# Performance work log

Hardware: AMD Instinct MI355X
Metric: run time of the kernel (lower is better)

## Reference

```python
import jax, jax.numpy as jnp
import numpy as np


def _sepconv1x1(x, dw, pw, b):
    # SeparableConv2D with kernel=1: depthwise 1x1 = per-channel scale, then pointwise matmul
    return jnp.einsum('nhwc,cd->nhwd', x * dw, pw) + b


def setup_inputs() -> dict:
    key = jax.random.key(0)
    ks = jax.random.split(key, 12)
    N, H, W, C_in, C_red = 4, 64, 64, 256, 64
    s = 0.05  # small init so softmax logits are well-conditioned
    return {
        'feature_maps': jax.random.normal(ks[0], (N, H, W, C_in), jnp.float32),
        'global_channel_output': jax.random.normal(ks[1], (N, H, W, C_in), jnp.float32),
        'dw_q': jax.random.normal(ks[2], (C_in,), jnp.float32) * s,
        'pw_q': jax.random.normal(ks[3], (C_in, C_red), jnp.float32) * s,
        'b_q': jnp.zeros((C_red,), jnp.float32),
        'dw_k': jax.random.normal(ks[4], (C_in,), jnp.float32) * s,
        'pw_k': jax.random.normal(ks[5], (C_in, C_red), jnp.float32) * s,
        'b_k': jnp.zeros((C_red,), jnp.float32),
        'dw_v': jax.random.normal(ks[6], (C_in,), jnp.float32) * s,
        'pw_v': jax.random.normal(ks[7], (C_in, C_red), jnp.float32) * s,
        'b_v': jnp.zeros((C_red,), jnp.float32),
        'dw_a': jax.random.normal(ks[8], (C_red,), jnp.float32) * s,
        'pw_a': jax.random.normal(ks[9], (C_red, C_in), jnp.float32) * s,
        'b_a': jnp.zeros((C_in,), jnp.float32),
    }


def reference(feature_maps, global_channel_output,
              dw_q, pw_q, b_q, dw_k, pw_k, b_k, dw_v, pw_v, b_v,
              dw_a, pw_a, b_a):
    N, H, W, _ = feature_maps.shape
    q = _sepconv1x1(feature_maps, dw_q, pw_q, b_q)  # [N,H,W,Cr]
    k = _sepconv1x1(feature_maps, dw_k, pw_k, b_k)
    v = _sepconv1x1(feature_maps, dw_v, pw_v, b_v)
    Cr = q.shape[-1]
    q = q.reshape(N, H * W, Cr)
    k = k.reshape(N, H * W, Cr)
    v = v.reshape(N, H * W, Cr)
    # tf.matmul(key, query, transpose_b=True): scores[i,j] = key_i . query_j
    scores = jnp.einsum('nic,njc->nij', k, q)  # [N,HW,HW]
    scores = jax.nn.softmax(scores, axis=-1)
    # tf.matmul(value, scores, transpose_a=True) -> [N,Cr,HW]
    att = jnp.einsum('nic,nij->ncj', v, scores)
    # faithful raw reshape (as in the original TF code) from [N,Cr,HW] to [N,H,W,Cr]
    att = att.reshape(N, H, W, Cr)
    att = _sepconv1x1(att, dw_a, pw_a, b_a)  # [N,H,W,C_in]
    return global_channel_output * att + global_channel_output
```

## Files before the change

### kernel.cpp

```cpp
#include <hip/hip_runtime.h>
#include <hip/hip_bf16.h>

typedef __attribute__((ext_vector_type(8))) __bf16 bf16x8;
typedef __attribute__((ext_vector_type(2))) __bf16 bf16x2;
typedef __attribute__((ext_vector_type(4))) float floatx4;
typedef __attribute__((ext_vector_type(4))) unsigned short us4;
typedef __attribute__((ext_vector_type(8))) unsigned short us8;
typedef __attribute__((ext_vector_type(4))) short s16x4;
typedef __attribute__((ext_vector_type(2))) unsigned int uint2v;
typedef __attribute__((ext_vector_type(4))) unsigned int uint4v;

#define MFMA16(A, B, C) __builtin_amdgcn_mfma_f32_16x16x32_bf16((A), (B), (C), 0, 0, 0)
#define MFMA1K(A, B, C) __builtin_amdgcn_mfma_f32_16x16x16bf16_1k((A), (B), (C), 0, 0, 0)

#define LOG2E 1.44269504088896340736f

#if __has_builtin(__builtin_amdgcn_exp2f)
#define EXP2F(x) __builtin_amdgcn_exp2f(x)
#else
#define EXP2F(x) exp2f(x)
#endif

static __device__ __forceinline__ unsigned short f2bfbits(float f) {
    __hip_bfloat16 h = __float2bfloat16(f);
    union { __hip_bfloat16 h; unsigned short u; } cv;
    cv.h = h;
    return cv.u;
}
static __device__ __forceinline__ unsigned int rne32(float f) {
    unsigned int u = __builtin_bit_cast(unsigned int, f);
    return u + 0x7fffu + ((u >> 16) & 1u);
}
static __device__ __forceinline__ unsigned short rne16(float f) {
    return (unsigned short)(rne32(f) >> 16);
}

#if __has_builtin(__builtin_amdgcn_cvt_pk_bf16_f32)
static __device__ __forceinline__ s16x4 pack4(float e0, float e1, float e2, float e3) {
    bf16x2 lo = __builtin_amdgcn_cvt_pk_bf16_f32(e0, e1);
    bf16x2 hi = __builtin_amdgcn_cvt_pk_bf16_f32(e2, e3);
    uint2v u = {__builtin_bit_cast(unsigned int, lo), __builtin_bit_cast(unsigned int, hi)};
    return __builtin_bit_cast(s16x4, u);
}
static __device__ __forceinline__ bf16x8 cvt8(floatx4 a, floatx4 b) {
    bf16x2 p0 = __builtin_amdgcn_cvt_pk_bf16_f32(a[0], a[1]);
    bf16x2 p1 = __builtin_amdgcn_cvt_pk_bf16_f32(a[2], a[3]);
    bf16x2 p2 = __builtin_amdgcn_cvt_pk_bf16_f32(b[0], b[1]);
    bf16x2 p3 = __builtin_amdgcn_cvt_pk_bf16_f32(b[2], b[3]);
    uint4v u = {__builtin_bit_cast(unsigned int, p0), __builtin_bit_cast(unsigned int, p1),
                __builtin_bit_cast(unsigned int, p2), __builtin_bit_cast(unsigned int, p3)};
    return __builtin_bit_cast(bf16x8, u);
}
#else
static __device__ __forceinline__ s16x4 pack4(float e0, float e1, float e2, float e3) {
    unsigned int pa = __builtin_amdgcn_perm(rne32(e1), rne32(e0), 0x07060302u);
    unsigned int pb = __builtin_amdgcn_perm(rne32(e3), rne32(e2), 0x07060302u);
    uint2v u = {pa, pb};
    return __builtin_bit_cast(s16x4, u);
}
static __device__ __forceinline__ bf16x8 cvt8(floatx4 a, floatx4 b) {
    us8 u;
#pragma unroll
    for (int i = 0; i < 4; i++) { u[i] = rne16(a[i]); u[4 + i] = rne16(b[i]); }
    return __builtin_bit_cast(bf16x8, u);
}
#endif

static __device__ __forceinline__ bf16x8 load_bf8(const __hip_bfloat16* p) {
    return *reinterpret_cast<const bf16x8*>(p);
}
static __device__ __forceinline__ float bf2f(unsigned short u) {
    unsigned int w = ((unsigned int)u) << 16;
    return __builtin_bit_cast(float, w);
}

static __device__ __forceinline__ void gld16(const void* g, void* l) {
    __builtin_amdgcn_global_load_lds(
        (const __attribute__((address_space(1))) unsigned int*)g,
        (__attribute__((address_space(3))) unsigned int*)l, 16, 0, 0);
}


__global__ __launch_bounds__(256) void proj_qkv(
    const float* __restrict__ x,
    const float* __restrict__ dwq, const float* __restrict__ pwq,
    const float* __restrict__ dwk, const float* __restrict__ pwk,
    const float* __restrict__ dwv, const float* __restrict__ pwv,
    const float* __restrict__ bqp, const float* __restrict__ bkp,
    const float* __restrict__ bvp,
    __hip_bfloat16* __restrict__ qf, __hip_bfloat16* __restrict__ kf,
    __hip_bfloat16* __restrict__ vf)
{
    __shared__ __hip_bfloat16 wle[16384];
    int b = blockIdx.x;
    int p = b >> 8;
    int tg = b & 255;
    int tid = threadIdx.x;

    const float* dw = (p == 0) ? dwq : ((p == 1) ? dwk : dwv);
    const float* pw = (p == 0) ? pwq : ((p == 1) ? pwk : pwv);
    float scale = (p == 1) ? LOG2E : 1.0f;

    {
        float dwc = dw[tid];
#pragma unroll
        for (int k = 0; k < 64; k++) {
            int idx = (k * 256 + tid) ^ ((k & 7) << 3);
            wle[idx] = __float2bfloat16(dwc * pw[tid * 64 + k] * scale);
        }
    }
    __syncthreads();

    int wv = tid >> 6;
    int wid = tg * 4 + wv;
    int lane = tid & 63;
    int l15 = lane & 15, quad = lane >> 4;

    floatx4 acc[4];
#pragma unroll
    for (int t = 0; t < 4; t++) acc[t] = (floatx4){0.f, 0.f, 0.f, 0.f};

    const float* xrow = x + (wid * 16 + l15) * 256 + quad * 8;
#pragma unroll
    for (int ks = 0; ks < 8; ks++) {
        floatx4 xa = *reinterpret_cast<const floatx4*>(xrow + ks * 32);
        floatx4 xb = *reinterpret_cast<const floatx4*>(xrow + ks * 32 + 4);
        bf16x8 a = cvt8(xa, xb);
#pragma unroll
        for (int t = 0; t < 4; t++) {
            int j0 = ((t * 16 + l15) * 256 + ks * 32 + quad * 8) ^ ((l15 & 7) << 3);
            bf16x8 bfr = *reinterpret_cast<const bf16x8*>(&wle[j0]);
            acc[t] = MFMA16(a, bfr, acc[t]);
        }
    }
    if (p < 2) {
        __hip_bfloat16* dst = (p == 0) ? qf : kf;
        const float* bias = (p == 0) ? bqp : bkp;
        float bscale = (p == 1) ? LOG2E : 1.0f;
#pragma unroll
        for (int t = 0; t < 4; t++) {
            float bsv = bias[t * 16 + l15] * bscale;
            int off0 = wid * 1024 + (t >> 1) * 512 +
                       (((((t & 1) << 1) | (l15 >> 3)) * 16 + quad * 4) * 8) + (l15 & 7);
#pragma unroll
            for (int r = 0; r < 4; r++)
                dst[off0 + r * 8] = __float2bfloat16(acc[t][r] + bsv);
        }
    } else {
#pragma unroll
        for (int t = 0; t < 4; t++) {
            float bsv = bvp[t * 16 + l15];
            us4 pk;
#pragma unroll
            for (int r = 0; r < 4; r++) pk[r] = f2bfbits(acc[t][r] + bsv);
            *reinterpret_cast<us4*>(vf + (wid * 4 + t) * 256 + lane * 4) = pk;
        }
    }
}

#define P1STEP(B0, B1, B2, B3) do {                                        \
    floatx4 z = (floatx4){0.f, 0.f, 0.f, 0.f};                             \
    floatx4 sA0 = MFMA16(a1, (B1), MFMA16(a0, (B0), z));                   \
    floatx4 sA1 = MFMA16(a1, (B3), MFMA16(a0, (B2), z));                   \
    floatx4 sB0 = MFMA16(a3, (B1), MFMA16(a2, (B0), z));                   \
    floatx4 sB1 = MFMA16(a3, (B3), MFMA16(a2, (B2), z));                   \
    _Pragma("unroll")                                                      \
    for (int r = 0; r < 4; r++) {                                          \
        lsA[r] += EXP2F(sA0[r]) + EXP2F(sA1[r]);                           \
        lsB[r] += EXP2F(sB0[r]) + EXP2F(sB1[r]);                           \
    }                                                                      \
} while (0)

__global__ __launch_bounds__(512) void pass1_rl(
    const __hip_bfloat16* __restrict__ qf, const __hip_bfloat16* __restrict__ kf,
    float* __restrict__ rl)
{
    int itg0 = blockIdx.x * 2;
    int n = itg0 >> 8;
    int jw = threadIdx.x >> 6;
    int lane = threadIdx.x & 63;
    int l15 = lane & 15, quad = lane >> 4;

    const __hip_bfloat16* kp = kf + itg0 * 1024 + lane * 8;
    bf16x8 a0 = load_bf8(kp);
    bf16x8 a1 = load_bf8(kp + 512);
    bf16x8 a2 = load_bf8(kp + 1024);
    bf16x8 a3 = load_bf8(kp + 1536);

    floatx4 lsA = (floatx4){0.f, 0.f, 0.f, 0.f};
    floatx4 lsB = (floatx4){0.f, 0.f, 0.f, 0.f};
    const __hip_bfloat16* qp0 = qf + (n * 256 + jw * 32) * 1024 + lane * 8;

    bf16x8 s0b0 = load_bf8(qp0);
    bf16x8 s0b1 = load_bf8(qp0 + 512);
    bf16x8 s0b2 = load_bf8(qp0 + 1024);
    bf16x8 s0b3 = load_bf8(qp0 + 1536);
    bf16x8 s1b0 = load_bf8(qp0 + 2048);
    bf16x8 s1b1 = load_bf8(qp0 + 2560);
    bf16x8 s1b2 = load_bf8(qp0 + 3072);
    bf16x8 s1b3 = load_bf8(qp0 + 3584);

    for (int it = 0; it < 16; it += 2) {
        bf16x8 n0 = load_bf8(qp0 + 4096);
        bf16x8 n1 = load_bf8(qp0 + 4608);
        bf16x8 n2 = load_bf8(qp0 + 5120);
        bf16x8 n3 = load_bf8(qp0 + 5632);
        P1STEP(s0b0, s0b1, s0b2, s0b3);
        s0b0 = n0; s0b1 = n1; s0b2 = n2; s0b3 = n3;
        bf16x8 m0 = load_bf8(qp0 + 6144);
        bf16x8 m1 = load_bf8(qp0 + 6656);
        bf16x8 m2 = load_bf8(qp0 + 7168);
        bf16x8 m3 = load_bf8(qp0 + 7680);
        P1STEP(s1b0, s1b1, s1b2, s1b3);
        s1b0 = m0; s1b1 = m1; s1b2 = m2; s1b3 = m3;
        qp0 += 4096;
    }
#pragma unroll
    for (int m = 1; m < 16; m <<= 1) {
#pragma unroll
        for (int r = 0; r < 4; r++) {
            lsA[r] += __shfl_xor(lsA[r], m, 64);
            lsB[r] += __shfl_xor(lsB[r], m, 64);
        }
    }
    __shared__ float red[8][32];
    if (l15 == 0) {
#pragma unroll
        for (int r = 0; r < 4; r++) {
            red[jw][quad * 4 + r] = lsA[r];
            red[jw][16 + quad * 4 + r] = lsB[r];
        }
    }
    __syncthreads();
    if (threadIdx.x < 32) {
        float tot = 0.f;
#pragma unroll
        for (int w = 0; w < 8; w++) tot += red[w][threadIdx.x];
        rl[itg0 * 16 + threadIdx.x] = 1.0f / tot;
    }
}

#define P2STEP(KA, KB, V0, V1, V2, V3, RLQ) do {                               \
    floatx4 z = (floatx4){0.f, 0.f, 0.f, 0.f};                                 \
    floatx4 s0 = MFMA16((KB), bq0b, MFMA16((KA), bq0a, z));                    \
    floatx4 s1 = MFMA16((KB), bq1b, MFMA16((KA), bq1a, z));                    \
    floatx4 s2 = MFMA16((KB), bq2b, MFMA16((KA), bq2a, z));                    \
    floatx4 s3 = MFMA16((KB), bq3b, MFMA16((KA), bq3a, z));                    \
    s16x4 p0 = pack4(EXP2F(s0[0]) * (RLQ)[0], EXP2F(s0[1]) * (RLQ)[1],         \
                     EXP2F(s0[2]) * (RLQ)[2], EXP2F(s0[3]) * (RLQ)[3]);        \
    s16x4 p1 = pack4(EXP2F(s1[0]) * (RLQ)[0], EXP2F(s1[1]) * (RLQ)[1],         \
                     EXP2F(s1[2]) * (RLQ)[2], EXP2F(s1[3]) * (RLQ)[3]);        \
    s16x4 p2 = pack4(EXP2F(s2[0]) * (RLQ)[0], EXP2F(s2[1]) * (RLQ)[1],         \
                     EXP2F(s2[2]) * (RLQ)[2], EXP2F(s2[3]) * (RLQ)[3]);        \
    s16x4 p3 = pack4(EXP2F(s3[0]) * (RLQ)[0], EXP2F(s3[1]) * (RLQ)[1],         \
                     EXP2F(s3[2]) * (RLQ)[2], EXP2F(s3[3]) * (RLQ)[3]);        \
    acc0[0] = MFMA1K(p0, (V0), acc0[0]);                                       \
    acc1[0] = MFMA1K(p1, (V0), acc1[0]);                                       \
    acc2[0] = MFMA1K(p2, (V0), acc2[0]);                                       \
    acc3[0] = MFMA1K(p3, (V0), acc3[0]);                                       \
    acc0[1] = MFMA1K(p0, (V1), acc0[1]);                                       \
    acc1[1] = MFMA1K(p1, (V1), acc1[1]);                                       \
    acc2[1] = MFMA1K(p2, (V1), acc2[1]);                                       \
    acc3[1] = MFMA1K(p3, (V1), acc3[1]);                                       \
    acc0[2] = MFMA1K(p0, (V2), acc0[2]);                                       \
    acc1[2] = MFMA1K(p1, (V2), acc1[2]);                                       \
    acc2[2] = MFMA1K(p2, (V2), acc2[2]);                                       \
    acc3[2] = MFMA1K(p3, (V2), acc3[2]);                                       \
    acc0[3] = MFMA1K(p0, (V3), acc0[3]);                                       \
    acc1[3] = MFMA1K(p1, (V3), acc1[3]);                                       \
    acc2[3] = MFMA1K(p2, (V3), acc2[3]);                                       \
    acc3[3] = MFMA1K(p3, (V3), acc3[3]);                                       \
} while (0)

__global__ __launch_bounds__(512) void pass2_att(
    const __hip_bfloat16* __restrict__ qf, const __hip_bfloat16* __restrict__ kf,
    const __hip_bfloat16* __restrict__ vf, const float* __restrict__ rl,
    unsigned short* __restrict__ attp)
{
    __shared__ char ldsbuf[2][8192];
    __shared__ float rl_lds[512];
    int b = blockIdx.x;
    int ih = b & 7;
    int jgrp = (b >> 3) & 7;
    int n = b >> 6;
    int tid = threadIdx.x;
    int w = tid >> 6;
    int lane = tid & 63;
    int l15 = lane & 15, quad = lane >> 4;
    int jt0 = jgrp * 32 + w * 4;

    int it0 = n * 256 + ih * 32;

    if (tid < 128)
        *reinterpret_cast<floatx4*>(&rl_lds[tid * 4]) =
            *reinterpret_cast<const floatx4*>(&rl[it0 * 16 + tid * 4]);

    const __hip_bfloat16* qp = qf + (n * 256 + jt0) * 1024 + lane * 8;
    bf16x8 bq0a = load_bf8(qp);
    bf16x8 bq0b = load_bf8(qp + 512);
    bf16x8 bq1a = load_bf8(qp + 1024);
    bf16x8 bq1b = load_bf8(qp + 1536);
    bf16x8 bq2a = load_bf8(qp + 2048);
    bf16x8 bq2b = load_bf8(qp + 2560);
    bf16x8 bq3a = load_bf8(qp + 3072);
    bf16x8 bq3b = load_bf8(qp + 3584);

    floatx4 acc0[4], acc1[4], acc2[4], acc3[4];
#pragma unroll
    for (int t = 0; t < 4; t++) {
        acc0[t] = (floatx4){0.f, 0.f, 0.f, 0.f};
        acc1[t] = (floatx4){0.f, 0.f, 0.f, 0.f};
        acc2[t] = (floatx4){0.f, 0.f, 0.f, 0.f};
        acc3[t] = (floatx4){0.f, 0.f, 0.f, 0.f};
    }

    const char* gbase = (w < 4) ? (const char*)(kf + it0 * 1024)
                                : (const char*)(vf + it0 * 1024);
    const char* gw = gbase + ((w >> 1) & 1) * 2048 + (w & 1) * 1024 + lane * 16;
    char* lw0 = &ldsbuf[0][w * 1024];
    char* lw1 = &ldsbuf[1][w * 1024];

    gld16(gw, lw0);
    __syncthreads();

    int cur = 0;
    for (int ph = 0; ph < 16; ph++) {
        if (ph < 15)
            gld16(gw + (ph + 1) * 4096, cur ? lw0 : lw1);
        const char* base = ldsbuf[cur];
#pragma unroll
        for (int t = 0; t < 2; t++) {
            bf16x8 a0 = *reinterpret_cast<const bf16x8*>(base + t * 2048 + lane * 16);
            bf16x8 a1 = *reinterpret_cast<const bf16x8*>(base + t * 2048 + 1024 + lane * 16);
            const char* vb = base + 4096 + t * 2048 + lane * 8;
            s16x4 v0 = *reinterpret_cast<const s16x4*>(vb);
            s16x4 v1 = *reinterpret_cast<const s16x4*>(vb + 512);
            s16x4 v2 = *reinterpret_cast<const s16x4*>(vb + 1024);
            s16x4 v3 = *reinterpret_cast<const s16x4*>(vb + 1536);
            floatx4 rlq = *reinterpret_cast<const floatx4*>(
                &rl_lds[(ph * 2 + t) * 16 + quad * 4]);
            P2STEP(a0, a1, v0, v1, v2, v3, rlq);
        }
        __syncthreads();
        cur ^= 1;
    }
    unsigned short* op0 = attp + ih * 1048576;
#pragma unroll
    for (int t = 0; t < 4; t++) {
        s16x4 k0 = pack4(acc0[t][0], acc0[t][1], acc0[t][2], acc0[t][3]);
        s16x4 k1 = pack4(acc1[t][0], acc1[t][1], acc1[t][2], acc1[t][3]);
        s16x4 k2 = pack4(acc2[t][0], acc2[t][1], acc2[t][2], acc2[t][3]);
        s16x4 k3 = pack4(acc3[t][0], acc3[t][1], acc3[t][2], acc3[t][3]);
        unsigned short* op = op0 + (n * 64 + t * 16 + l15) * 4096 + jt0 * 16 + quad * 4;
        *reinterpret_cast<s16x4*>(op) = k0;
        *reinterpret_cast<s16x4*>(op + 16) = k1;
        *reinterpret_cast<s16x4*>(op + 32) = k2;
        *reinterpret_cast<s16x4*>(op + 48) = k3;
    }
}

template<int NPART>
__global__ __launch_bounds__(256) void final_out(
    const unsigned short* __restrict__ attp, const float* __restrict__ gco,
    const float* __restrict__ dwa, const float* __restrict__ pwa,
    const float* __restrict__ ba, float* __restrict__ out)
{
    int b = blockIdx.x;
    int n = b >> 9;
    int hh = (b >> 3) & 63;
    int w0 = (b & 7) << 3;
    __shared__ float g[512];
    int tid = threadIdx.x;
    const unsigned short* ap = attp + (n * 64 + hh) * 4096 + w0 * 64;
    {
        int jj0 = tid * 2;
        float v0 = 0.f, v1 = 0.f;
#pragma unroll
        for (int ph = 0; ph < NPART; ph++) {
            unsigned int u = *reinterpret_cast<const unsigned int*>(ap + ph * 1048576 + jj0);
            v0 += bf2f((unsigned short)(u & 0xffffu));
            v1 += bf2f((unsigned short)(u >> 16));
        }
        g[jj0] = v0 * dwa[jj0 & 63];
        g[jj0 + 1] = v1 * dwa[(jj0 + 1) & 63];
    }
    __syncthreads();
    float acc[8];
#pragma unroll
    for (int w = 0; w < 8; w++) acc[w] = 0.f;
    for (int cc = 0; cc < 64; cc++) {
        float p = pwa[cc * 256 + tid];
#pragma unroll
        for (int w = 0; w < 8; w++) acc[w] += g[w * 64 + cc] * p;
    }
    float bb = ba[tid];
#pragma unroll
    for (int w = 0; w < 8; w++) {
        int pos = (n * 64 + hh) * 64 + w0 + w;
        float gv = gco[pos * 256 + tid];
        out[pos * 256 + tid] = gv * (acc[w] + bb) + gv;
    }
}

extern "C" void kernel_launch(void* const* d_in, const int* in_sizes, int n_in,
                              void* d_out, int out_size, void* d_ws, size_t ws_size,
                              hipStream_t stream) {
    const float* x   = (const float*)d_in[0];
    const float* gco = (const float*)d_in[1];
    const float* dwq = (const float*)d_in[2];
    const float* pwq = (const float*)d_in[3];
    const float* bq  = (const float*)d_in[4];
    const float* dwk = (const float*)d_in[5];
    const float* pwk = (const float*)d_in[6];
    const float* bk  = (const float*)d_in[7];
    const float* dwv = (const float*)d_in[8];
    const float* pwv = (const float*)d_in[9];
    const float* bv  = (const float*)d_in[10];
    const float* dwa = (const float*)d_in[11];
    const float* pwa = (const float*)d_in[12];
    const float* ba  = (const float*)d_in[13];
    float* out = (float*)d_out;

    char* ws = (char*)d_ws;
    __hip_bfloat16* qf  = (__hip_bfloat16*)(ws + 98304);
    __hip_bfloat16* kf  = (__hip_bfloat16*)(ws + 2195456);
    __hip_bfloat16* vf  = (__hip_bfloat16*)(ws + 4292608);
    float*          rlb = (float*)(ws + 6389760);
    unsigned short* attp = (unsigned short*)(ws + 8486912);

    proj_qkv<<<768, 256, 0, stream>>>(x, dwq, pwq, dwk, pwk, dwv, pwv,
                                      bq, bk, bv, qf, kf, vf);
    pass1_rl<<<512, 512, 0, stream>>>(qf, kf, rlb);
    pass2_att<<<256, 512, 0, stream>>>(qf, kf, vf, rlb, attp);
    final_out<8><<<2048, 256, 0, stream>>>(attp, gco, dwa, pwa, ba, out);
}
```

Measured before the change: 167.2 us.

## Fuse all stages into one cooperative persistent kernel with grid syncs

Replaces the four separate launches (projection, row-sum pass, attention pass, output) with one cooperative kernel of 256 blocks that uses grid.sync between stages, and redistributes per-block work (4 key tiles per block in pass1, 2 projection tiles per wave). The goal is to remove inter-kernel launch gaps and tail effects. The fallback path, used only if the cooperative launch fails, switches pass2 to a 512-block grid with half the query tiles per wave. The risk is that 256 blocks underfill the GPU and grid barriers add their own cost.

```diff
diff --git a/kernel.cpp b/kernel.cpp
--- a/kernel.cpp
+++ b/kernel.cpp
@@ -1,5 +1,8 @@
 #include <hip/hip_runtime.h>
 #include <hip/hip_bf16.h>
+#include <hip/hip_cooperative_groups.h>
+
+namespace cg = cooperative_groups;
 
 typedef __attribute__((ext_vector_type(8))) __bf16 bf16x8;
 typedef __attribute__((ext_vector_type(2))) __bf16 bf16x2;
@@ -81,164 +84,24 @@
 }
 
 
-__global__ __launch_bounds__(256) void proj_qkv(
-    const float* __restrict__ x,
-    const float* __restrict__ dwq, const float* __restrict__ pwq,
-    const float* __restrict__ dwk, const float* __restrict__ pwk,
-    const float* __restrict__ dwv, const float* __restrict__ pwv,
-    const float* __restrict__ bqp, const float* __restrict__ bkp,
-    const float* __restrict__ bvp,
-    __hip_bfloat16* __restrict__ qf, __hip_bfloat16* __restrict__ kf,
-    __hip_bfloat16* __restrict__ vf)
-{
-    __shared__ __hip_bfloat16 wle[16384];
-    int b = blockIdx.x;
-    int p = b >> 8;
-    int tg = b & 255;
-    int tid = threadIdx.x;
-
-    const float* dw = (p == 0) ? dwq : ((p == 1) ? dwk : dwv);
-    const float* pw = (p == 0) ? pwq : ((p == 1) ? pwk : pwv);
-    float scale = (p == 1) ? LOG2E : 1.0f;
-
-    {
-        float dwc = dw[tid];
-#pragma unroll
-        for (int k = 0; k < 64; k++) {
-            int idx = (k * 256 + tid) ^ ((k & 7) << 3);
-            wle[idx] = __float2bfloat16(dwc * pw[tid * 64 + k] * scale);
-        }
-    }
-    __syncthreads();
-
-    int wv = tid >> 6;
-    int wid = tg * 4 + wv;
-    int lane = tid & 63;
-    int l15 = lane & 15, quad = lane >> 4;
-
-    floatx4 acc[4];
-#pragma unroll
-    for (int t = 0; t < 4; t++) acc[t] = (floatx4){0.f, 0.f, 0.f, 0.f};
-
-    const float* xrow = x + (wid * 16 + l15) * 256 + quad * 8;
-#pragma unroll
-    for (int ks = 0; ks < 8; ks++) {
-        floatx4 xa = *reinterpret_cast<const floatx4*>(xrow + ks * 32);
-        floatx4 xb = *reinterpret_cast<const floatx4*>(xrow + ks * 32 + 4);
-        bf16x8 a = cvt8(xa, xb);
-#pragma unroll
-        for (int t = 0; t < 4; t++) {
-            int j0 = ((t * 16 + l15) * 256 + ks * 32 + quad * 8) ^ ((l15 & 7) << 3);
-            bf16x8 bfr = *reinterpret_cast<const bf16x8*>(&wle[j0]);
-            acc[t] = MFMA16(a, bfr, acc[t]);
-        }
-    }
-    if (p < 2) {
-        __hip_bfloat16* dst = (p == 0) ? qf : kf;
-        const float* bias = (p == 0) ? bqp : bkp;
-        float bscale = (p == 1) ? LOG2E : 1.0f;
-#pragma unroll
-        for (int t = 0; t < 4; t++) {
-            float bsv = bias[t * 16 + l15] * bscale;
-            int off0 = wid * 1024 + (t >> 1) * 512 +
-                       (((((t & 1) << 1) | (l15 >> 3)) * 16 + quad * 4) * 8) + (l15 & 7);
-#pragma unroll
-            for (int r = 0; r < 4; r++)
-                dst[off0 + r * 8] = __float2bfloat16(acc[t][r] + bsv);
-        }
-    } else {
-#pragma unroll
-        for (int t = 0; t < 4; t++) {
-            float bsv = bvp[t * 16 + l15];
-            us4 pk;
-#pragma unroll
-            for (int r = 0; r < 4; r++) pk[r] = f2bfbits(acc[t][r] + bsv);
-            *reinterpret_cast<us4*>(vf + (wid * 4 + t) * 256 + lane * 4) = pk;
-        }
-    }
-}
-
-#define P1STEP(B0, B1, B2, B3) do {                                        \
+#define P1STEP4(B0, B1, B2, B3) do {                                       \
     floatx4 z = (floatx4){0.f, 0.f, 0.f, 0.f};                             \
     floatx4 sA0 = MFMA16(a1, (B1), MFMA16(a0, (B0), z));                   \
     floatx4 sA1 = MFMA16(a1, (B3), MFMA16(a0, (B2), z));                   \
     floatx4 sB0 = MFMA16(a3, (B1), MFMA16(a2, (B0), z));                   \
     floatx4 sB1 = MFMA16(a3, (B3), MFMA16(a2, (B2), z));                   \
+    floatx4 sC0 = MFMA16(a5, (B1), MFMA16(a4, (B0), z));                   \
+    floatx4 sC1 = MFMA16(a5, (B3), MFMA16(a4, (B2), z));                   \
+    floatx4 sD0 = MFMA16(a7, (B1), MFMA16(a6, (B0), z));                   \
+    floatx4 sD1 = MFMA16(a7, (B3), MFMA16(a6, (B2), z));                   \
     _Pragma("unroll")                                                      \
     for (int r = 0; r < 4; r++) {                                          \
-        lsA[r] += EXP2F(sA0[r]) + EXP2F(sA1[r]);                           \
-        lsB[r] += EXP2F(sB0[r]) + EXP2F(sB1[r]);                           \
+        ls0[r] += EXP2F(sA0[r]) + EXP2F(sA1[r]);                           \
+        ls1[r] += EXP2F(sB0[r]) + EXP2F(sB1[r]);                           \
+        ls2[r] += EXP2F(sC0[r]) + EXP2F(sC1[r]);                           \
+        ls3[r] += EXP2F(sD0[r]) + EXP2F(sD1[r]);                           \
     }                                                                      \
 } while (0)
-
-__global__ __launch_bounds__(512) void pass1_rl(
-    const __hip_bfloat16* __restrict__ qf, const __hip_bfloat16* __restrict__ kf,
-    float* __restrict__ rl)
-{
-    int itg0 = blockIdx.x * 2;
-    int n = itg0 >> 8;
-    int jw = threadIdx.x >> 6;
-    int lane = threadIdx.x & 63;
-    int l15 = lane & 15, quad = lane >> 4;
-
-    const __hip_bfloat16* kp = kf + itg0 * 1024 + lane * 8;
-    bf16x8 a0 = load_bf8(kp);
-    bf16x8 a1 = load_bf8(kp + 512);
-    bf16x8 a2 = load_bf8(kp + 1024);
-    bf16x8 a3 = load_bf8(kp + 1536);
-
-    floatx4 lsA = (floatx4){0.f, 0.f, 0.f, 0.f};
-    floatx4 lsB = (floatx4){0.f, 0.f, 0.f, 0.f};
-    const __hip_bfloat16* qp0 = qf + (n * 256 + jw * 32) * 1024 + lane * 8;
-
-    bf16x8 s0b0 = load_bf8(qp0);
-    bf16x8 s0b1 = load_bf8(qp0 + 512);
-    bf16x8 s0b2 = load_bf8(qp0 + 1024);
-    bf16x8 s0b3 = load_bf8(qp0 + 1536);
-    bf16x8 s1b0 = load_bf8(qp0 + 2048);
-    bf16x8 s1b1 = load_bf8(qp0 + 2560);
-    bf16x8 s1b2 = load_bf8(qp0 + 3072);
-    bf16x8 s1b3 = load_bf8(qp0 + 3584);
-
-    for (int it = 0; it < 16; it += 2) {
-        bf16x8 n0 = load_bf8(qp0 + 4096);
-        bf16x8 n1 = load_bf8(qp0 + 4608);
-        bf16x8 n2 = load_bf8(qp0 + 5120);
-        bf16x8 n3 = load_bf8(qp0 + 5632);
-        P1STEP(s0b0, s0b1, s0b2, s0b3);
-        s0b0 = n0; s0b1 = n1; s0b2 = n2; s0b3 = n3;
-        bf16x8 m0 = load_bf8(qp0 + 6144);
-        bf16x8 m1 = load_bf8(qp0 + 6656);
-        bf16x8 m2 = load_bf8(qp0 + 7168);
-        bf16x8 m3 = load_bf8(qp0 + 7680);
-        P1STEP(s1b0, s1b1, s1b2, s1b3);
-        s1b0 = m0; s1b1 = m1; s1b2 = m2; s1b3 = m3;
-        qp0 += 4096;
-    }
-#pragma unroll
-    for (int m = 1; m < 16; m <<= 1) {
-#pragma unroll
-        for (int r = 0; r < 4; r++) {
-            lsA[r] += __shfl_xor(lsA[r], m, 64);
-            lsB[r] += __shfl_xor(lsB[r], m, 64);
-        }
-    }
-    __shared__ float red[8][32];
-    if (l15 == 0) {
-#pragma unroll
-        for (int r = 0; r < 4; r++) {
-            red[jw][quad * 4 + r] = lsA[r];
-            red[jw][16 + quad * 4 + r] = lsB[r];
-        }
-    }
-    __syncthreads();
-    if (threadIdx.x < 32) {
-        float tot = 0.f;
-#pragma unroll
-        for (int w = 0; w < 8; w++) tot += red[w][threadIdx.x];
-        rl[itg0 * 16 + threadIdx.x] = 1.0f / tot;
-    }
-}
 
 #define P2STEP(KA, KB, V0, V1, V2, V3, RLQ) do {                               \
     floatx4 z = (floatx4){0.f, 0.f, 0.f, 0.f};                                 \
@@ -272,6 +135,463 @@
     acc3[3] = MFMA1K(p3, (V3), acc3[3]);                                       \
 } while (0)
 
+__global__ __launch_bounds__(512) void fused_all(
+    const float* __restrict__ x, const float* __restrict__ gco,
+    const float* __restrict__ dwq, const float* __restrict__ pwq, const float* __restrict__ bqp,
+    const float* __restrict__ dwk, const float* __restrict__ pwk, const float* __restrict__ bkp,
+    const float* __restrict__ dwv, const float* __restrict__ pwv, const float* __restrict__ bvp,
+    const float* __restrict__ dwa, const float* __restrict__ pwa, const float* __restrict__ ba,
+    __hip_bfloat16* __restrict__ qf, __hip_bfloat16* __restrict__ kf,
+    __hip_bfloat16* __restrict__ vf, float* __restrict__ rl,
+    unsigned short* __restrict__ attp, float* __restrict__ out)
+{
+    cg::grid_group grid = cg::this_grid();
+    __shared__ __align__(16) char smem[34816];
+    int bid = blockIdx.x;
+    int tid = threadIdx.x;
+    int w = tid >> 6;
+    int lane = tid & 63;
+    int l15 = lane & 15, quad = lane >> 4;
+
+    {
+        __hip_bfloat16* wle = (__hip_bfloat16*)smem;
+        int c = tid & 255, kh = tid >> 8;
+        int tile_l = w >> 1;
+        int wid = bid * 4 + tile_l;
+        int t0 = (w & 1) * 2;
+        const float* xrow = x + (wid * 16 + l15) * 256 + quad * 8;
+        for (int p = 0; p < 3; p++) {
+            const float* dw = (p == 0) ? dwq : ((p == 1) ? dwk : dwv);
+            const float* pw = (p == 0) ? pwq : ((p == 1) ? pwk : pwv);
+            float scale = (p == 1) ? LOG2E : 1.0f;
+            {
+                float dwc = dw[c];
+#pragma unroll
+                for (int k2 = 0; k2 < 32; k2++) {
+                    int k = kh * 32 + k2;
+                    int idx = (k * 256 + c) ^ ((k & 7) << 3);
+                    wle[idx] = __float2bfloat16(dwc * pw[c * 64 + k] * scale);
+                }
+            }
+            __syncthreads();
+            floatx4 acc[2];
+            acc[0] = (floatx4){0.f, 0.f, 0.f, 0.f};
+            acc[1] = (floatx4){0.f, 0.f, 0.f, 0.f};
+#pragma unroll
+            for (int ks = 0; ks < 8; ks++) {
+                floatx4 xa = *reinterpret_cast<const floatx4*>(xrow + ks * 32);
+                floatx4 xb = *reinterpret_cast<const floatx4*>(xrow + ks * 32 + 4);
+                bf16x8 a = cvt8(xa, xb);
+#pragma unroll
+                for (int tt = 0; tt < 2; tt++) {
+                    int t = t0 + tt;
+                    int j0 = ((t * 16 + l15) * 256 + ks * 32 + quad * 8) ^ ((l15 & 7) << 3);
+                    bf16x8 bfr = *reinterpret_cast<const bf16x8*>(&wle[j0]);
+                    acc[tt] = MFMA16(a, bfr, acc[tt]);
+                }
+            }
+            if (p < 2) {
+                __hip_bfloat16* dst = (p == 0) ? qf : kf;
+                const float* bias = (p == 0) ? bqp : bkp;
+                float bscale = (p == 1) ? LOG2E : 1.0f;
+#pragma unroll
+                for (int tt = 0; tt < 2; tt++) {
+                    int t = t0 + tt;
+                    float bsv = bias[t * 16 + l15] * bscale;
+                    int off0 = wid * 1024 + (t >> 1) * 512 +
+                               (((((t & 1) << 1) | (l15 >> 3)) * 16 + quad * 4) * 8) + (l15 & 7);
+#pragma unroll
+                    for (int r = 0; r < 4; r++)
+                        dst[off0 + r * 8] = __float2bfloat16(acc[tt][r] + bsv);
+                }
+            } else {
+#pragma unroll
+                for (int tt = 0; tt < 2; tt++) {
+                    int t = t0 + tt;
+                    float bsv = bvp[t * 16 + l15];
+                    us4 pk;
+#pragma unroll
+                    for (int r = 0; r < 4; r++) pk[r] = f2bfbits(acc[tt][r] + bsv);
+                    *reinterpret_cast<us4*>(vf + (wid * 4 + t) * 256 + lane * 4) = pk;
+                }
+            }
+            __syncthreads();
+        }
+    }
+    grid.sync();
+
+    {
+        int itg0 = bid * 4;
+        int n = bid >> 6;
+        const __hip_bfloat16* kp = kf + itg0 * 1024 + lane * 8;
+        bf16x8 a0 = load_bf8(kp);
+        bf16x8 a1 = load_bf8(kp + 512);
+        bf16x8 a2 = load_bf8(kp + 1024);
+        bf16x8 a3 = load_bf8(kp + 1536);
+        bf16x8 a4 = load_bf8(kp + 2048);
+        bf16x8 a5 = load_bf8(kp + 2560);
+        bf16x8 a6 = load_bf8(kp + 3072);
+        bf16x8 a7 = load_bf8(kp + 3584);
+
+        floatx4 ls0 = (floatx4){0.f, 0.f, 0.f, 0.f};
+        floatx4 ls1 = (floatx4){0.f, 0.f, 0.f, 0.f};
+        floatx4 ls2 = (floatx4){0.f, 0.f, 0.f, 0.f};
+        floatx4 ls3 = (floatx4){0.f, 0.f, 0.f, 0.f};
+        const __hip_bfloat16* qp0 = qf + (n * 256 + w * 32) * 1024 + lane * 8;
+
+        bf16x8 s0b0 = load_bf8(qp0);
+        bf16x8 s0b1 = load_bf8(qp0 + 512);
+        bf16x8 s0b2 = load_bf8(qp0 + 1024);
+        bf16x8 s0b3 = load_bf8(qp0 + 1536);
+        bf16x8 s1b0 = load_bf8(qp0 + 2048);
+        bf16x8 s1b1 = load_bf8(qp0 + 2560);
+        bf16x8 s1b2 = load_bf8(qp0 + 3072);
+        bf16x8 s1b3 = load_bf8(qp0 + 3584);
+
+        for (int it = 0; it < 16; it += 2) {
+            bf16x8 n0 = load_bf8(qp0 + 4096);
+            bf16x8 n1 = load_bf8(qp0 + 4608);
+            bf16x8 n2 = load_bf8(qp0 + 5120);
+            bf16x8 n3 = load_bf8(qp0 + 5632);
+            P1STEP4(s0b0, s0b1, s0b2, s0b3);
+            s0b0 = n0; s0b1 = n1; s0b2 = n2; s0b3 = n3;
+            bf16x8 m0 = load_bf8(qp0 + 6144);
+            bf16x8 m1 = load_bf8(qp0 + 6656);
+            bf16x8 m2 = load_bf8(qp0 + 7168);
+            bf16x8 m3 = load_bf8(qp0 + 7680);
+            P1STEP4(s1b0, s1b1, s1b2, s1b3);
+            s1b0 = m0; s1b1 = m1; s1b2 = m2; s1b3 = m3;
+            qp0 += 4096;
+        }
+#pragma unroll
+        for (int m = 1; m < 16; m <<= 1) {
+#pragma unroll
+            for (int r = 0; r < 4; r++) {
+                ls0[r] += __shfl_xor(ls0[r], m, 64);
+                ls1[r] += __shfl_xor(ls1[r], m, 64);
+                ls2[r] += __shfl_xor(ls2[r], m, 64);
+                ls3[r] += __shfl_xor(ls3[r], m, 64);
+            }
+        }
+        float* red = (float*)(smem + 32768);
+        if (l15 == 0) {
+#pragma unroll
+            for (int r = 0; r < 4; r++) {
+                red[w * 64 + quad * 4 + r]      = ls0[r];
+                red[w * 64 + 16 + quad * 4 + r] = ls1[r];
+                red[w * 64 + 32 + quad * 4 + r] = ls2[r];
+                red[w * 64 + 48 + quad * 4 + r] = ls3[r];
+            }
+        }
+        __syncthreads();
+        if (tid < 64) {
+            float tot = 0.f;
+#pragma unroll
+            for (int w2 = 0; w2 < 8; w2++) tot += red[w2 * 64 + tid];
+            rl[bid * 64 + tid] = 1.0f / tot;
+        }
+    }
+    grid.sync();
+
+    {
+        char* ldsb = smem;
+        float* rl_lds = (float*)(smem + 16384);
+        int ih = bid & 7;
+        int jgrp = (bid >> 3) & 7;
+        int n = bid >> 6;
+        int jt0 = jgrp * 32 + w * 4;
+
+        int it0 = n * 256 + ih * 32;
+        if (tid < 128)
+            *reinterpret_cast<floatx4*>(&rl_lds[tid * 4]) =
+                *reinterpret_cast<const floatx4*>(&rl[it0 * 16 + tid * 4]);
+
+        const __hip_bfloat16* qp = qf + (n * 256 + jt0) * 1024 + lane * 8;
+        bf16x8 bq0a = load_bf8(qp);
+        bf16x8 bq0b = load_bf8(qp + 512);
+        bf16x8 bq1a = load_bf8(qp + 1024);
+        bf16x8 bq1b = load_bf8(qp + 1536);
+        bf16x8 bq2a = load_bf8(qp + 2048);
+        bf16x8 bq2b = load_bf8(qp + 2560);
+        bf16x8 bq3a = load_bf8(qp + 3072);
+        bf16x8 bq3b = load_bf8(qp + 3584);
+
+        floatx4 acc0[4], acc1[4], acc2[4], acc3[4];
+#pragma unroll
+        for (int t = 0; t < 4; t++) {
+            acc0[t] = (floatx4){0.f, 0.f, 0.f, 0.f};
+            acc1[t] = (floatx4){0.f, 0.f, 0.f, 0.f};
+            acc2[t] = (floatx4){0.f, 0.f, 0.f, 0.f};
+            acc3[t] = (floatx4){0.f, 0.f, 0.f, 0.f};
+        }
+
+        const char* gbase = (w < 4) ? (const char*)(kf + it0 * 1024)
+                                    : (const char*)(vf + it0 * 1024);
+        const char* gw = gbase + ((w >> 1) & 1) * 2048 + (w & 1) * 1024 + lane * 16;
+        char* lw0 = ldsb + w * 1024;
+        char* lw1 = ldsb + 8192 + w * 1024;
+
+        gld16(gw, lw0);
+        __syncthreads();
+
+        int cur = 0;
+        for (int ph = 0; ph < 16; ph++) {
+            if (ph < 15)
+                gld16(gw + (ph + 1) * 4096, cur ? lw0 : lw1);
+            const char* base = ldsb + cur * 8192;
+#pragma unroll
+            for (int t = 0; t < 2; t++) {
+                bf16x8 a0 = *reinterpret_cast<const bf16x8*>(base + t * 2048 + lane * 16);
+                bf16x8 a1 = *reinterpret_cast<const bf16x8*>(base + t * 2048 + 1024 + lane * 16);
+                const char* vb = base + 4096 + t * 2048 + lane * 8;
+                s16x4 v0 = *reinterpret_cast<const s16x4*>(vb);
+                s16x4 v1 = *reinterpret_cast<const s16x4*>(vb + 512);
+                s16x4 v2 = *reinterpret_cast<const s16x4*>(vb + 1024);
+                s16x4 v3 = *reinterpret_cast<const s16x4*>(vb + 1536);
+                floatx4 rlq = *reinterpret_cast<const floatx4*>(
+                    &rl_lds[(ph * 2 + t) * 16 + quad * 4]);
+                P2STEP(a0, a1, v0, v1, v2, v3, rlq);
+            }
+            __syncthreads();
+            cur ^= 1;
+        }
+        unsigned short* op0 = attp + ih * 1048576;
+#pragma unroll
+        for (int t = 0; t < 4; t++) {
+            s16x4 k0 = pack4(acc0[t][0], acc0[t][1], acc0[t][2], acc0[t][3]);
+            s16x4 k1 = pack4(acc1[t][0], acc1[t][1], acc1[t][2], acc1[t][3]);
+            s16x4 k2 = pack4(acc2[t][0], acc2[t][1], acc2[t][2], acc2[t][3]);
+            s16x4 k3 = pack4(acc3[t][0], acc3[t][1], acc3[t][2], acc3[t][3]);
+            unsigned short* op = op0 + (n * 64 + t * 16 + l15) * 4096 + jt0 * 16 + quad * 4;
+            *reinterpret_cast<s16x4*>(op) = k0;
+            *reinterpret_cast<s16x4*>(op + 16) = k1;
+            *reinterpret_cast<s16x4*>(op + 32) = k2;
+            *reinterpret_cast<s16x4*>(op + 48) = k3;
+        }
+    }
+    grid.sync();
+
+    {
+        float* gg = (float*)smem;
+        int sub = tid >> 8;
+        int t256 = tid & 255;
+        for (int rnd = 0; rnd < 4; rnd++) {
+            int o = bid * 8 + rnd * 2 + sub;
+            int n = o >> 9;
+            int hh = (o >> 3) & 63;
+            int w0 = (o & 7) << 3;
+            const unsigned short* ap = attp + (n * 64 + hh) * 4096 + w0 * 64;
+            float* g = gg + sub * 512;
+            {
+                int jj0 = t256 * 2;
+                float v0 = 0.f, v1 = 0.f;
+#pragma unroll
+                for (int ph = 0; ph < 8; ph++) {
+                    unsigned int u = *reinterpret_cast<const unsigned int*>(ap + ph * 1048576 + jj0);
+                    v0 += bf2f((unsigned short)(u & 0xffffu));
+                    v1 += bf2f((unsigned short)(u >> 16));
+                }
+                g[jj0] = v0 * dwa[jj0 & 63];
+                g[jj0 + 1] = v1 * dwa[(jj0 + 1) & 63];
+            }
+            __syncthreads();
+            float acc[8];
+#pragma unroll
+            for (int ww = 0; ww < 8; ww++) acc[ww] = 0.f;
+            for (int cc = 0; cc < 64; cc++) {
+                float p = pwa[cc * 256 + t256];
+#pragma unroll
+                for (int ww = 0; ww < 8; ww++) acc[ww] += g[ww * 64 + cc] * p;
+            }
+            float bb = ba[t256];
+#pragma unroll
+            for (int ww = 0; ww < 8; ww++) {
+                int pos = (n * 64 + hh) * 64 + w0 + ww;
+                float gv = gco[pos * 256 + t256];
+                out[pos * 256 + t256] = gv * (acc[ww] + bb) + gv;
+            }
+            __syncthreads();
+        }
+    }
+}
+
+__global__ __launch_bounds__(256) void proj_qkv(
+    const float* __restrict__ x,
+    const float* __restrict__ dwq, const float* __restrict__ pwq,
+    const float* __restrict__ dwk, const float* __restrict__ pwk,
+    const float* __restrict__ dwv, const float* __restrict__ pwv,
+    const float* __restrict__ bqp, const float* __restrict__ bkp,
+    const float* __restrict__ bvp,
+    __hip_bfloat16* __restrict__ qf, __hip_bfloat16* __restrict__ kf,
+    __hip_bfloat16* __restrict__ vf)
+{
+    __shared__ __hip_bfloat16 wle[16384];
+    int b = blockIdx.x;
+    int p = b >> 8;
+    int tg = b & 255;
+    int tid = threadIdx.x;
+
+    const float* dw = (p == 0) ? dwq : ((p == 1) ? dwk : dwv);
+    const float* pw = (p == 0) ? pwq : ((p == 1) ? pwk : pwv);
+    float scale = (p == 1) ? LOG2E : 1.0f;
+
+    {
+        float dwc = dw[tid];
+#pragma unroll
+        for (int k = 0; k < 64; k++) {
+            int idx = (k * 256 + tid) ^ ((k & 7) << 3);
+            wle[idx] = __float2bfloat16(dwc * pw[tid * 64 + k] * scale);
+        }
+    }
+    __syncthreads();
+
+    int wv = tid >> 6;
+    int wid = tg * 4 + wv;
+    int lane = tid & 63;
+    int l15 = lane & 15, quad = lane >> 4;
+
+    floatx4 acc[4];
+#pragma unroll
+    for (int t = 0; t < 4; t++) acc[t] = (floatx4){0.f, 0.f, 0.f, 0.f};
+
+    const float* xrow = x + (wid * 16 + l15) * 256 + quad * 8;
+#pragma unroll
+    for (int ks = 0; ks < 8; ks++) {
+        floatx4 xa = *reinterpret_cast<const floatx4*>(xrow + ks * 32);
+        floatx4 xb = *reinterpret_cast<const floatx4*>(xrow + ks * 32 + 4);
+        bf16x8 a = cvt8(xa, xb);
+#pragma unroll
+        for (int t = 0; t < 4; t++) {
+            int j0 = ((t * 16 + l15) * 256 + ks * 32 + quad * 8) ^ ((l15 & 7) << 3);
+            bf16x8 bfr = *reinterpret_cast<const bf16x8*>(&wle[j0]);
+            acc[t] = MFMA16(a, bfr, acc[t]);
+        }
+    }
+    if (p < 2) {
+        __hip_bfloat16* dst = (p == 0) ? qf : kf;
+        const float* bias = (p == 0) ? bqp : bkp;
+        float bscale = (p == 1) ? LOG2E : 1.0f;
+#pragma unroll
+        for (int t = 0; t < 4; t++) {
+            float bsv = bias[t * 16 + l15] * bscale;
+            int off0 = wid * 1024 + (t >> 1) * 512 +
+                       (((((t & 1) << 1) | (l15 >> 3)) * 16 + quad * 4) * 8) + (l15 & 7);
+#pragma unroll
+            for (int r = 0; r < 4; r++)
+                dst[off0 + r * 8] = __float2bfloat16(acc[t][r] + bsv);
+        }
+    } else {
+#pragma unroll
+        for (int t = 0; t < 4; t++) {
+            float bsv = bvp[t * 16 + l15];
+            us4 pk;
+#pragma unroll
+            for (int r = 0; r < 4; r++) pk[r] = f2bfbits(acc[t][r] + bsv);
+            *reinterpret_cast<us4*>(vf + (wid * 4 + t) * 256 + lane * 4) = pk;
+        }
+    }
+}
+
+#define P1STEP(B0, B1, B2, B3) do {                                        \
+    floatx4 z = (floatx4){0.f, 0.f, 0.f, 0.f};                             \
+    floatx4 sA0 = MFMA16(a1, (B1), MFMA16(a0, (B0), z));                   \
+    floatx4 sA1 = MFMA16(a1, (B3), MFMA16(a0, (B2), z));                   \
+    floatx4 sB0 = MFMA16(a3, (B1), MFMA16(a2, (B0), z));                   \
+    floatx4 sB1 = MFMA16(a3, (B3), MFMA16(a2, (B2), z));                   \
+    _Pragma("unroll")                                                      \
+    for (int r = 0; r < 4; r++) {                                          \
+        lsA[r] += EXP2F(sA0[r]) + EXP2F(sA1[r]);                           \
+        lsB[r] += EXP2F(sB0[r]) + EXP2F(sB1[r]);                           \
+    }                                                                      \
+} while (0)
+
+__global__ __launch_bounds__(512) void pass1_rl(
+    const __hip_bfloat16* __restrict__ qf, const __hip_bfloat16* __restrict__ kf,
+    float* __restrict__ rl)
+{
+    int itg0 = blockIdx.x * 2;
+    int n = itg0 >> 8;
+    int jw = threadIdx.x >> 6;
+    int lane = threadIdx.x & 63;
+    int l15 = lane & 15, quad = lane >> 4;
+
+    const __hip_bfloat16* kp = kf + itg0 * 1024 + lane * 8;
+    bf16x8 a0 = load_bf8(kp);
+    bf16x8 a1 = load_bf8(kp + 512);
+    bf16x8 a2 = load_bf8(kp + 1024);
+    bf16x8 a3 = load_bf8(kp + 1536);
+
+    floatx4 lsA = (floatx4){0.f, 0.f, 0.f, 0.f};
+    floatx4 lsB = (floatx4){0.f, 0.f, 0.f, 0.f};
+    const __hip_bfloat16* qp0 = qf + (n * 256 + jw * 32) * 1024 + lane * 8;
+
+    bf16x8 s0b0 = load_bf8(qp0);
+    bf16x8 s0b1 = load_bf8(qp0 + 512);
+    bf16x8 s0b2 = load_bf8(qp0 + 1024);
+    bf16x8 s0b3 = load_bf8(qp0 + 1536);
+    bf16x8 s1b0 = load_bf8(qp0 + 2048);
+    bf16x8 s1b1 = load_bf8(qp0 + 2560);
+    bf16x8 s1b2 = load_bf8(qp0 + 3072);
+    bf16x8 s1b3 = load_bf8(qp0 + 3584);
+
+    for (int it = 0; it < 16; it += 2) {
+        bf16x8 n0 = load_bf8(qp0 + 4096);
+        bf16x8 n1 = load_bf8(qp0 + 4608);
+        bf16x8 n2 = load_bf8(qp0 + 5120);
+        bf16x8 n3 = load_bf8(qp0 + 5632);
+        P1STEP(s0b0, s0b1, s0b2, s0b3);
+        s0b0 = n0; s0b1 = n1; s0b2 = n2; s0b3 = n3;
+        bf16x8 m0 = load_bf8(qp0 + 6144);
+        bf16x8 m1 = load_bf8(qp0 + 6656);
+        bf16x8 m2 = load_bf8(qp0 + 7168);
+        bf16x8 m3 = load_bf8(qp0 + 7680);
+        P1STEP(s1b0, s1b1, s1b2, s1b3);
+        s1b0 = m0; s1b1 = m1; s1b2 = m2; s1b3 = m3;
+        qp0 += 4096;
+    }
+#pragma unroll
+    for (int m = 1; m < 16; m <<= 1) {
+#pragma unroll
+        for (int r = 0; r < 4; r++) {
+            lsA[r] += __shfl_xor(lsA[r], m, 64);
+            lsB[r] += __shfl_xor(lsB[r], m, 64);
+        }
+    }
+    __shared__ float red[8][32];
+    if (l15 == 0) {
+#pragma unroll
+        for (int r = 0; r < 4; r++) {
+            red[jw][quad * 4 + r] = lsA[r];
+            red[jw][16 + quad * 4 + r] = lsB[r];
+        }
+    }
+    __syncthreads();
+    if (threadIdx.x < 32) {
+        float tot = 0.f;
+#pragma unroll
+        for (int w = 0; w < 8; w++) tot += red[w][threadIdx.x];
+        rl[itg0 * 16 + threadIdx.x] = 1.0f / tot;
+    }
+}
+
+#define P2STEP2(KA, KB, V0, V1, V2, V3, RLQ) do {                              \
+    floatx4 z = (floatx4){0.f, 0.f, 0.f, 0.f};                                 \
+    floatx4 s0 = MFMA16((KB), bq0b, MFMA16((KA), bq0a, z));                    \
+    floatx4 s1 = MFMA16((KB), bq1b, MFMA16((KA), bq1a, z));                    \
+    s16x4 p0 = pack4(EXP2F(s0[0]) * (RLQ)[0], EXP2F(s0[1]) * (RLQ)[1],         \
+                     EXP2F(s0[2]) * (RLQ)[2], EXP2F(s0[3]) * (RLQ)[3]);        \
+    s16x4 p1 = pack4(EXP2F(s1[0]) * (RLQ)[0], EXP2F(s1[1]) * (RLQ)[1],         \
+                     EXP2F(s1[2]) * (RLQ)[2], EXP2F(s1[3]) * (RLQ)[3]);        \
+    acc0[0] = MFMA1K(p0, (V0), acc0[0]);                                       \
+    acc1[0] = MFMA1K(p1, (V0), acc1[0]);                                       \
+    acc0[1] = MFMA1K(p0, (V1), acc0[1]);                                       \
+    acc1[1] = MFMA1K(p1, (V1), acc1[1]);                                       \
+    acc0[2] = MFMA1K(p0, (V2), acc0[2]);                                       \
+    acc1[2] = MFMA1K(p1, (V2), acc1[2]);                                       \
+    acc0[3] = MFMA1K(p0, (V3), acc0[3]);                                       \
+    acc1[3] = MFMA1K(p1, (V3), acc1[3]);                                       \
+} while (0)
+
 __global__ __launch_bounds__(512) void pass2_att(
     const __hip_bfloat16* __restrict__ qf, const __hip_bfloat16* __restrict__ kf,
     const __hip_bfloat16* __restrict__ vf, const float* __restrict__ rl,
@@ -281,16 +601,15 @@
     __shared__ float rl_lds[512];
     int b = blockIdx.x;
     int ih = b & 7;
-    int jgrp = (b >> 3) & 7;
-    int n = b >> 6;
+    int jgrp = (b >> 3) & 15;
+    int n = b >> 7;
     int tid = threadIdx.x;
     int w = tid >> 6;
     int lane = tid & 63;
     int l15 = lane & 15, quad = lane >> 4;
-    int jt0 = jgrp * 32 + w * 4;
+    int jt0 = jgrp * 16 + w * 2;
 
     int it0 = n * 256 + ih * 32;
-
     if (tid < 128)
         *reinterpret_cast<floatx4*>(&rl_lds[tid * 4]) =
             *reinterpret_cast<const floatx4*>(&rl[it0 * 16 + tid * 4]);
@@ -300,18 +619,12 @@
     bf16x8 bq0b = load_bf8(qp + 512);
     bf16x8 bq1a = load_bf8(qp + 1024);
     bf16x8 bq1b = load_bf8(qp + 1536);
-    bf16x8 bq2a = load_bf8(qp + 2048);
-    bf16x8 bq2b = load_bf8(qp + 2560);
-    bf16x8 bq3a = load_bf8(qp + 3072);
-    bf16x8 bq3b = load_bf8(qp + 3584);
-
-    floatx4 acc0[4], acc1[4], acc2[4], acc3[4];
+
+    floatx4 acc0[4], acc1[4];
 #pragma unroll
     for (int t = 0; t < 4; t++) {
         acc0[t] = (floatx4){0.f, 0.f, 0.f, 0.f};
         acc1[t] = (floatx4){0.f, 0.f, 0.f, 0.f};
-        acc2[t] = (floatx4){0.f, 0.f, 0.f, 0.f};
-        acc3[t] = (floatx4){0.f, 0.f, 0.f, 0.f};
     }
 
     const char* gbase = (w < 4) ? (const char*)(kf + it0 * 1024)
@@ -339,7 +652,7 @@
             s16x4 v3 = *reinterpret_cast<const s16x4*>(vb + 1536);
             floatx4 rlq = *reinterpret_cast<const floatx4*>(
                 &rl_lds[(ph * 2 + t) * 16 + quad * 4]);
-            P2STEP(a0, a1, v0, v1, v2, v3, rlq);
+            P2STEP2(a0, a1, v0, v1, v2, v3, rlq);
         }
         __syncthreads();
         cur ^= 1;
@@ -349,13 +662,9 @@
     for (int t = 0; t < 4; t++) {
         s16x4 k0 = pack4(acc0[t][0], acc0[t][1], acc0[t][2], acc0[t][3]);
         s16x4 k1 = pack4(acc1[t][0], acc1[t][1], acc1[t][2], acc1[t][3]);
-        s16x4 k2 = pack4(acc2[t][0], acc2[t][1], acc2[t][2], acc2[t][3]);
-        s16x4 k3 = pack4(acc3[t][0], acc3[t][1], acc3[t][2], acc3[t][3]);
         unsigned short* op = op0 + (n * 64 + t * 16 + l15) * 4096 + jt0 * 16 + quad * 4;
         *reinterpret_cast<s16x4*>(op) = k0;
         *reinterpret_cast<s16x4*>(op + 16) = k1;
-        *reinterpret_cast<s16x4*>(op + 32) = k2;
-        *reinterpret_cast<s16x4*>(op + 48) = k3;
     }
 }
 
@@ -428,9 +737,23 @@
     float*          rlb = (float*)(ws + 6389760);
     unsigned short* attp = (unsigned short*)(ws + 8486912);
 
-    proj_qkv<<<768, 256, 0, stream>>>(x, dwq, pwq, dwk, pwk, dwv, pwv,
-                                      bq, bk, bv, qf, kf, vf);
-    pass1_rl<<<512, 512, 0, stream>>>(qf, kf, rlb);
-    pass2_att<<<256, 512, 0, stream>>>(qf, kf, vf, rlb, attp);
-    final_out<8><<<2048, 256, 0, stream>>>(attp, gco, dwa, pwa, ba, out);
-}
+    void* args[] = {
+        (void*)&x, (void*)&gco,
+        (void*)&dwq, (void*)&pwq, (void*)&bq,
+        (void*)&dwk, (void*)&pwk, (void*)&bk,
+        (void*)&dwv, (void*)&pwv, (void*)&bv,
+        (void*)&dwa, (void*)&pwa, (void*)&ba,
+        (void*)&qf, (void*)&kf, (void*)&vf,
+        (void*)&rlb, (void*)&attp, (void*)&out
+    };
+    hipError_t err = hipLaunchCooperativeKernel(
+        (void*)fused_all, dim3(256), dim3(512), args, 0, stream);
+
+    if (err != hipSuccess) {
+        proj_qkv<<<768, 256, 0, stream>>>(x, dwq, pwq, dwk, pwk, dwv, pwv,
+                                          bq, bk, bv, qf, kf, vf);
+        pass1_rl<<<512, 512, 0, stream>>>(qf, kf, rlb);
+        pass2_att<<<512, 512, 0, stream>>>(qf, kf, vf, rlb, attp);
+        final_out<8><<<2048, 256, 0, stream>>>(attp, gco, dwa, pwa, ba, out);
+    }
+}
```

After: 266.3 us. +59.2%, slower.
